# Kernel optimization log

Hardware: AMD Instinct MI355X
Metric: run time of the kernel (lower is better)

## Reference

```python
import jax, jax.numpy as jnp
import numpy as np

EMBED_DIM = 1024
HEAD_NUM = 16
HEAD_DIM = EMBED_DIM // HEAD_NUM
T, B, S = 2048, 4, 2048


def setup_inputs() -> dict:
    key = jax.random.key(0)
    ks = jax.random.split(key, 11)
    s = 0.02
    return {
        "query": jax.random.normal(ks[0], (T, B, EMBED_DIM), jnp.float32),
        "key": jax.random.normal(ks[1], (S, B, EMBED_DIM), jnp.float32),
        "value": jax.random.normal(ks[2], (S, B, EMBED_DIM), jnp.float32),
        "q_proj_weight": jax.random.normal(ks[3], (EMBED_DIM, EMBED_DIM), jnp.float32) * s,
        "k_proj_weight": jax.random.normal(ks[4], (EMBED_DIM, EMBED_DIM), jnp.float32) * s,
        "v_proj_weight": jax.random.normal(ks[5], (EMBED_DIM, EMBED_DIM), jnp.float32) * s,
        "in_proj_bias": jax.random.normal(ks[6], (3 * EMBED_DIM,), jnp.float32) * s,
        "bias_k": jax.random.normal(ks[7], (1, 1, EMBED_DIM), jnp.float32) * s,
        "bias_v": jax.random.normal(ks[8], (1, 1, EMBED_DIM), jnp.float32) * s,
        "out_proj_weight": jax.random.normal(ks[9], (EMBED_DIM, EMBED_DIM), jnp.float32) * s,
        "out_proj_bias": jax.random.normal(ks[10], (EMBED_DIM,), jnp.float32) * s,
    }


def reference(query, key, value, q_proj_weight, k_proj_weight, v_proj_weight,
              in_proj_bias, bias_k, bias_v, out_proj_weight, out_proj_bias):
    t, b, e = query.shape
    h, hd = HEAD_NUM, HEAD_DIM
    scaling = float(hd) ** -0.5
    # input projections (F.linear: x @ W.T + b)
    q = (query @ q_proj_weight.T + in_proj_bias[:e]) * scaling          # [T,B,E]
    k = key @ k_proj_weight.T + in_proj_bias[e:2 * e]                   # [S,B,E]
    v = value @ v_proj_weight.T + in_proj_bias[2 * e:]                  # [S,B,E]
    # append bias_k / bias_v token along the sequence dim
    k = jnp.concatenate([k, jnp.broadcast_to(bias_k, (1, b, e))], axis=0)  # [S+1,B,E]
    v = jnp.concatenate([v, jnp.broadcast_to(bias_v, (1, b, e))], axis=0)  # [S+1,B,E]
    # split heads: [L, B, E] -> [B*H, L, hd]
    q = q.reshape(t, b * h, hd).transpose(1, 0, 2)
    k = k.reshape(-1, b * h, hd).transpose(1, 0, 2)
    v = v.reshape(-1, b * h, hd).transpose(1, 0, 2)
    # full O(T*S) attention, as in the original bmm->softmax->bmm
    weights = jax.nn.softmax(jnp.einsum('nqd,nkd->nqk', q, k), axis=-1)  # [B*H,T,S+1]
    out = jnp.einsum('nqk,nkd->nqd', weights, v)                         # [B*H,T,hd]
    out = out.transpose(1, 0, 2).reshape(t, b, e)
    out = out @ out_proj_weight.T + out_proj_bias
    avg_weights = weights.sum(axis=1) / h                                # [B*H,S+1]
    return out, avg_weights
```

## Files before the change

kernel.cpp:

```cpp
#include <hip/hip_runtime.h>

#define T_DIM 2048
#define B_DIM 4
#define S_DIM 2048
#define E_DIM 1024
#define H_NUM 16
#define HD    64
#define NH    64
#define SP1   2049
#define SPAD  2112
#define NCHUNK 33
#define NTOKE ((size_t)T_DIM * B_DIM * E_DIM)

typedef short bf16x8 __attribute__((ext_vector_type(8)));
typedef short bf16x4 __attribute__((ext_vector_type(4)));
typedef float f32x4  __attribute__((ext_vector_type(4)));
typedef float f32x16 __attribute__((ext_vector_type(16)));
typedef unsigned int u32;

#define QSCALE 0.18033688011112042f

#if __has_builtin(__builtin_amdgcn_exp2f)
__device__ __forceinline__ float exp2_fast(float x) { return __builtin_amdgcn_exp2f(x); }
#else
__device__ __forceinline__ float exp2_fast(float x) { return __expf(x * 0.6931471805599453f); }
#endif

__device__ __forceinline__ unsigned short f2bf(float x) {
    union { float f; unsigned int u; } v; v.f = x;
    unsigned int r = v.u + 0x7FFFu + ((v.u >> 16) & 1u);
    return (unsigned short)(r >> 16);
}

__device__ __forceinline__ u32 cvtpk_bf16(float lo, float hi) {
    u32 r;
    asm("v_cvt_pk_bf16_f32 %0, %1, %2" : "=v"(r) : "v"(lo), "v"(hi));
    return r;
}
__device__ __forceinline__ void plswap(u32& a, u32& b) {
    asm("v_permlane32_swap_b32 %0, %1" : "+v"(a), "+v"(b));
}

__device__ __forceinline__ void load_lds16(const void* g, void* l) {
    __builtin_amdgcn_global_load_lds(
        (const __attribute__((address_space(1))) unsigned int*)g,
        (__attribute__((address_space(3))) unsigned int*)l, 16, 0, 0);
}

__global__ __launch_bounds__(256)
void cvt_all(const float* __restrict__ q, const float* __restrict__ k,
             const float* __restrict__ v, const float* __restrict__ w0,
             const float* __restrict__ w1, const float* __restrict__ w2,
             const float* __restrict__ w3, short* __restrict__ indst,
             short* __restrict__ wdst, short* __restrict__ k_h,
             short* __restrict__ v_h, const float* __restrict__ bias_k,
             const float* __restrict__ bias_v)
{
    const int y = blockIdx.y;
    if (y < 3) {
        const float* src = (y == 0) ? q : (y == 1) ? k : v;
        short* d = indst + (size_t)y * NTOKE;
        const size_t i = (size_t)blockIdx.x * 256 + threadIdx.x;
        const float4* s = reinterpret_cast<const float4*>(src) + i * 2;
        float4 a = s[0], b = s[1];
        uint4 o;
        o.x = cvtpk_bf16(a.x, a.y); o.y = cvtpk_bf16(a.z, a.w);
        o.z = cvtpk_bf16(b.x, b.y); o.w = cvtpk_bf16(b.z, b.w);
        *(reinterpret_cast<uint4*>(d) + i) = o;
    } else {
        const size_t gi = (size_t)blockIdx.x * 256 + threadIdx.x;
        const size_t per = (size_t)E_DIM * E_DIM / 8;
        if (gi < 4 * per) {
            const int wsel = (int)(gi / per);
            const size_t i = gi % per;
            const float* src = (wsel == 0) ? w0 : (wsel == 1) ? w1 : (wsel == 2) ? w2 : w3;
            short* d = wdst + (size_t)wsel * E_DIM * E_DIM;
            const float4* s = reinterpret_cast<const float4*>(src) + i * 2;
            float4 a = s[0], b = s[1];
            uint4 o;
            o.x = cvtpk_bf16(a.x, a.y); o.y = cvtpk_bf16(a.z, a.w);
            o.z = cvtpk_bf16(b.x, b.y); o.w = cvtpk_bf16(b.z, b.w);
            *(reinterpret_cast<uint4*>(d) + i) = o;
        } else {
            const size_t fi = gi - 4 * per;
            if (fi < (size_t)(SPAD - S_DIM) * NH * HD) {
                const int d   = (int)(fi & 63);
                const int row = (int)((fi >> 6) & 63);
                const int n   = (int)(fi >> 12);
                short bk = 0, bv = 0;
                if (row == 0) {
                    bk = (short)f2bf(bias_k[(n & 15) * HD + d]);
                    bv = (short)f2bf(bias_v[(n & 15) * HD + d]);
                }
                const size_t idx = ((size_t)n * SPAD + S_DIM + row) * HD + d;
                k_h[idx] = bk;
                v_h[idx] = bv;
            }
        }
    }
}

template<int MODE>
__global__ __launch_bounds__(256, 4)
void gemm_bf16(const short* __restrict__ Abase, const short* __restrict__ Wall,
               const float* __restrict__ biasAll, void* __restrict__ outp)
{
    __shared__ short As[128][64];
    __shared__ short Bs[128][64];
    const int bm = blockIdx.x, bn = blockIdx.y;
    const int z = (MODE == 0) ? blockIdx.z : 0;
    const short* Az = Abase + (MODE == 0 ? (size_t)z * NTOKE : 0);
    const short* W  = Wall + (size_t)z * E_DIM * E_DIM;
    const float* bias = biasAll + z * E_DIM;

    const int tid = threadIdx.x;
    const int l = tid & 63, w = tid >> 6;
    const int wr = w >> 1, wc = w & 1;
    const int lr = l & 15, lg = l >> 4;
    const int srow = tid >> 3, scol = (tid & 7) * 8;

    f32x4 acc[4][4] = {};

    for (int k0 = 0; k0 < E_DIM; k0 += 64) {
#pragma unroll
        for (int r = 0; r < 4; ++r) {
            const int row = r * 32 + srow;
            const short* ga;
            if (MODE == 3) {
                const int m = bm * 128 + row;
                ga = Az + ((size_t)((m & 3) * 16 + (k0 >> 6)) * T_DIM + (m >> 2)) * HD + scol;
            } else {
                ga = Az + (size_t)(bm * 128 + row) * E_DIM + k0 + scol;
            }
            load_lds16(ga, &As[row][scol]);
            load_lds16(W + (size_t)(bn * 128 + row) * E_DIM + k0 + scol, &Bs[row][scol]);
        }
        __syncthreads();

        __builtin_amdgcn_s_setprio(1);
#pragma unroll
        for (int c = 0; c < 2; ++c) {
            bf16x8 af[4], bf[4];
#pragma unroll
            for (int mi = 0; mi < 4; ++mi)
                af[mi] = *reinterpret_cast<const bf16x8*>(&As[wr * 64 + mi * 16 + lr][c * 32 + lg * 8]);
#pragma unroll
            for (int ni = 0; ni < 4; ++ni)
                bf[ni] = *reinterpret_cast<const bf16x8*>(&Bs[wc * 64 + ni * 16 + lr][c * 32 + lg * 8]);
#pragma unroll
            for (int mi = 0; mi < 4; ++mi)
#pragma unroll
                for (int ni = 0; ni < 4; ++ni)
                    acc[mi][ni] = __builtin_amdgcn_mfma_f32_16x16x32_bf16(
                        af[mi], bf[ni], acc[mi][ni], 0, 0, 0);
        }
        __builtin_amdgcn_s_setprio(0);
        __syncthreads();
    }

#pragma unroll
    for (int mi = 0; mi < 4; ++mi)
#pragma unroll
        for (int ni = 0; ni < 4; ++ni) {
            const int colg = bn * 128 + wc * 64 + ni * 16 + lr;
            const float bv = bias[colg];
#pragma unroll
            for (int r = 0; r < 4; ++r) {
                const int m = bm * 128 + wr * 64 + mi * 16 + lg * 4 + r;
                float v = acc[mi][ni][r] + bv;
                if (MODE == 3) {
                    ((float*)outp)[(size_t)m * E_DIM + colg] = v;
                } else {
                    if (z == 0) v *= QSCALE;
                    const int seq = m >> 2, b = m & 3;
                    const int head = colg >> 6, d = colg & 63;
                    const int sd = (z == 0) ? T_DIM : SPAD;
                    short* ob = (short*)outp;
                    if (z == 1) ob += (size_t)NH * T_DIM * HD;
                    else if (z == 2) ob += (size_t)NH * T_DIM * HD + (size_t)NH * SPAD * HD;
                    ob[((size_t)(b * 16 + head) * sd + seq) * HD + d] = (short)f2bf(v);
                }
            }
        }
}

__global__ __launch_bounds__(512, 4)
void attn_mfma(const short* __restrict__ q_h, const short* __restrict__ k_h,
               const short* __restrict__ v_h, short* __restrict__ o_h,
               float* __restrict__ m_arr, float* __restrict__ l_arr)
{
    __shared__ short KsD[2][64 * 64];
    __shared__ short VtD[2][64 * 64];

    const int id = blockIdx.x;
    const int xcd = id & 7, slot = id >> 3;
    const int n = xcd * 8 + (slot >> 3);
    const int q0 = (slot & 7) * 256;

    const int tid = threadIdx.x, l = tid & 63, w = tid >> 6;
    const int ql = l & 31;
    const int hi = l >> 5;
    const int qrow = q0 + w * 32 + ql;

    const int krow = tid >> 3, kcg = tid & 7;
    const int kswz = (kcg * 16) ^ ((krow & 7) << 4);
    const int sp = tid & 31, dq = tid >> 5;

    const short* kbase = k_h + (size_t)n * SPAD * HD;
    const short* vbase = v_h + (size_t)n * SPAD * HD;

    bf16x8 aq0, aq1, aq2, aq3;
    {
        const short* qp = q_h + ((size_t)n * T_DIM + qrow) * HD + hi * 8;
        aq0 = *(const bf16x8*)(qp);
        aq1 = *(const bf16x8*)(qp + 16);
        aq2 = *(const bf16x8*)(qp + 32);
        aq3 = *(const bf16x8*)(qp + 48);
    }

    bf16x8 pk  = *(const bf16x8*)(kbase + (size_t)krow * HD + kcg * 8);
    bf16x4 pva = *(const bf16x4*)(vbase + (size_t)(2 * sp) * HD + dq * 4);
    bf16x4 pvb = *(const bf16x4*)(vbase + (size_t)(2 * sp + 1) * HD + dq * 4);
    {
        char* KsB = (char*)KsD[0];
        char* VtB = (char*)VtD[0];
        *(bf16x8*)(KsB + krow * 128 + kswz) = pk;
#pragma unroll
        for (int j = 0; j < 4; ++j) {
            u32 pkd = (u32)(unsigned short)pva[j] | ((u32)(unsigned short)pvb[j] << 16);
            const int d = dq * 4 + j;
            *(u32*)(VtB + d * 128 + ((4 * sp) ^ ((d & 7) << 4))) = pkd;
        }
    }
    __syncthreads();

    float m_run = 0.0f;
    float l_run = 0.0f;
    f32x16 accA, accB;
#pragma unroll
    for (int r = 0; r < 16; ++r) { accA[r] = 0.f; accB[r] = 0.f; }

    for (int kc = 0; kc < NCHUNK; ++kc) {
        const char* KsB = (const char*)KsD[kc & 1];
        const char* VtB = (const char*)VtD[kc & 1];
        const bool more = (kc + 1 < NCHUNK);

        if (more) {
            const int s0n = (kc + 1) * 64;
            pk  = *(const bf16x8*)(kbase + (size_t)(s0n + krow) * HD + kcg * 8);
            pva = *(const bf16x4*)(vbase + (size_t)(s0n + 2 * sp) * HD + dq * 4);
            pvb = *(const bf16x4*)(vbase + (size_t)(s0n + 2 * sp + 1) * HD + dq * 4);
        }

        f32x16 sc0, sc1;
        const float nm = -m_run;
#pragma unroll
        for (int r = 0; r < 16; ++r) { sc0[r] = nm; sc1[r] = nm; }
        __builtin_amdgcn_s_setprio(1);
#pragma unroll
        for (int sl = 0; sl < 4; ++sl) {
            const int cb = ((sl * 32) + hi * 16) ^ ((ql & 7) << 4);
            bf16x8 kf0 = *(const bf16x8*)(KsB + ql * 128 + cb);
            bf16x8 kf1 = *(const bf16x8*)(KsB + (32 + ql) * 128 + cb);
            bf16x8 qf = (sl == 0) ? aq0 : (sl == 1) ? aq1 : (sl == 2) ? aq2 : aq3;
            sc0 = __builtin_amdgcn_mfma_f32_32x32x16_bf16(kf0, qf, sc0, 0, 0, 0);
            sc1 = __builtin_amdgcn_mfma_f32_32x32x16_bf16(kf1, qf, sc1, 0, 0, 0);
        }
        __builtin_amdgcn_s_setprio(0);

        const int s0 = kc * 64;
        if (s0 + 64 > SP1) {
#pragma unroll
            for (int r = 0; r < 16; ++r) {
                const int key = (r & 3) + 8 * (r >> 2) + 4 * hi;
                if (s0 + key >= SP1)      sc0[r] = -1e30f;
                if (s0 + 32 + key >= SP1) sc1[r] = -1e30f;
            }
        }

        float mv[16];
#pragma unroll
        for (int r = 0; r < 16; ++r) mv[r] = fmaxf(sc0[r], sc1[r]);
#pragma unroll
        for (int s = 8; s > 0; s >>= 1)
#pragma unroll
            for (int r = 0; r < s; ++r) mv[r] = fmaxf(mv[r], mv[r + s]);
        const float mx = fmaxf(mv[0], __shfl_xor(mv[0], 32));
        if (!__all(mx <= 8.0f)) {
            const float sh = fmaxf(mx, 0.0f);
            const float fac = exp2_fast(-sh);
            l_run *= fac;
#pragma unroll
            for (int r = 0; r < 16; ++r) {
                accA[r] *= fac; accB[r] *= fac;
                sc0[r] -= sh;   sc1[r] -= sh;
            }
            m_run += sh;
        }
        float p0[16], p1[16];
#pragma unroll
        for (int r = 0; r < 16; ++r) p0[r] = exp2_fast(sc0[r]);
#pragma unroll
        for (int r = 0; r < 16; ++r) p1[r] = exp2_fast(sc1[r]);
        float sv[16];
#pragma unroll
        for (int r = 0; r < 16; ++r) sv[r] = p0[r] + p1[r];
#pragma unroll
        for (int s = 8; s > 0; s >>= 1)
#pragma unroll
            for (int r = 0; r < s; ++r) sv[r] += sv[r + s];
        l_run += sv[0] + __shfl_xor(sv[0], 32);

        union PF { u32 u[4]; bf16x8 v; };
        PF pf0, pf1, pf2, pf3;
        {
            u32 a0 = cvtpk_bf16(p0[0], p0[1]),   b0 = cvtpk_bf16(p0[4], p0[5]);   plswap(a0, b0);
            u32 a1 = cvtpk_bf16(p0[2], p0[3]),   b1 = cvtpk_bf16(p0[6], p0[7]);   plswap(a1, b1);
            u32 a2 = cvtpk_bf16(p0[8], p0[9]),   b2 = cvtpk_bf16(p0[12], p0[13]); plswap(a2, b2);
            u32 a3 = cvtpk_bf16(p0[10], p0[11]), b3 = cvtpk_bf16(p0[14], p0[15]); plswap(a3, b3);
            pf0.u[0] = a0; pf0.u[1] = a1; pf0.u[2] = b0; pf0.u[3] = b1;
            pf1.u[0] = a2; pf1.u[1] = a3; pf1.u[2] = b2; pf1.u[3] = b3;
            u32 c0 = cvtpk_bf16(p1[0], p1[1]),   d0_ = cvtpk_bf16(p1[4], p1[5]);   plswap(c0, d0_);
            u32 c1 = cvtpk_bf16(p1[2], p1[3]),   d1_ = cvtpk_bf16(p1[6], p1[7]);   plswap(c1, d1_);
            u32 c2 = cvtpk_bf16(p1[8], p1[9]),   d2_ = cvtpk_bf16(p1[12], p1[13]); plswap(c2, d2_);
            u32 c3 = cvtpk_bf16(p1[10], p1[11]), d3_ = cvtpk_bf16(p1[14], p1[15]); plswap(c3, d3_);
            pf2.u[0] = c0; pf2.u[1] = c1; pf2.u[2] = d0_; pf2.u[3] = d1_;
            pf3.u[0] = c2; pf3.u[1] = c3; pf3.u[2] = d2_; pf3.u[3] = d3_;
        }

        __builtin_amdgcn_s_setprio(1);
#pragma unroll
        for (int ksl = 0; ksl < 4; ++ksl) {
            const int cb = ((ksl * 32) + hi * 16) ^ ((ql & 7) << 4);
            bf16x8 vf0 = *(const bf16x8*)(VtB + ql * 128 + cb);
            bf16x8 vf1 = *(const bf16x8*)(VtB + (32 + ql) * 128 + cb);
            const bf16x8 pv = (ksl == 0) ? pf0.v : (ksl == 1) ? pf1.v : (ksl == 2) ? pf2.v : pf3.v;
            accA = __builtin_amdgcn_mfma_f32_32x32x16_bf16(vf0, pv, accA, 0, 0, 0);
            accB = __builtin_amdgcn_mfma_f32_32x32x16_bf16(vf1, pv, accB, 0, 0, 0);
        }
        __builtin_amdgcn_s_setprio(0);

        if (more) {
            char* KsN = (char*)KsD[(kc & 1) ^ 1];
            char* VtN = (char*)VtD[(kc & 1) ^ 1];
            *(bf16x8*)(KsN + krow * 128 + kswz) = pk;
#pragma unroll
            for (int j = 0; j < 4; ++j) {
                u32 pkd = (u32)(unsigned short)pva[j] | ((u32)(unsigned short)pvb[j] << 16);
                const int d = dq * 4 + j;
                *(u32*)(VtN + d * 128 + ((4 * sp) ^ ((d & 7) << 4))) = pkd;
            }
            __syncthreads();
        }
    }

    const float il = 1.0f / l_run;
    short* orow = o_h + ((size_t)n * T_DIM + qrow) * HD;
#pragma unroll
    for (int rq = 0; rq < 4; ++rq) {
        uint2 st;
        st.x = cvtpk_bf16(accA[rq * 4 + 0] * il, accA[rq * 4 + 1] * il);
        st.y = cvtpk_bf16(accA[rq * 4 + 2] * il, accA[rq * 4 + 3] * il);
        *(uint2*)(orow + rq * 8 + hi * 4) = st;
        uint2 st2;
        st2.x = cvtpk_bf16(accB[rq * 4 + 0] * il, accB[rq * 4 + 1] * il);
        st2.y = cvtpk_bf16(accB[rq * 4 + 2] * il, accB[rq * 4 + 3] * il);
        *(uint2*)(orow + 32 + rq * 8 + hi * 4) = st2;
    }
    if (hi == 0) {
        m_arr[n * T_DIM + qrow] = m_run;
        l_arr[n * T_DIM + qrow] = l_run;
    }
}

__global__ __launch_bounds__(256)
void colsum_mfma(const short* __restrict__ q_h, const short* __restrict__ k_h,
                 const float* __restrict__ m_arr, const float* __restrict__ l_arr,
                 float* __restrict__ avg_out)
{
    __shared__ short Qs[2][64][72];
    __shared__ float msh[2][64];
    __shared__ float lih[2][64];

    const int id = blockIdx.x;
    const int xcd = id & 7, slot = id >> 3;
    const int n = xcd * 8 + slot / 33;
    const int s0 = (slot % 33) * 64;

    const int tid = threadIdx.x, l = tid & 63, w = tid >> 6;
    const int lr = l & 15, lg = l >> 4;
    const int qr = tid >> 3, qcg = tid & 7;

    const short* qbase = q_h + (size_t)n * T_DIM * HD;

    bf16x8 ak[2];
#pragma unroll
    for (int c = 0; c < 2; ++c)
        ak[c] = *reinterpret_cast<const bf16x8*>(
            k_h + ((size_t)n * SPAD + s0 + w * 16 + lr) * HD + c * 32 + lg * 8);

    bf16x8 qa = *(const bf16x8*)(qbase + (size_t)qr * HD + qcg * 8);
    bf16x8 qb = *(const bf16x8*)(qbase + (size_t)(32 + qr) * HD + qcg * 8);
    float mlv = 0.f;
    if (tid < 64) mlv = m_arr[n * T_DIM + tid];
    else if (tid < 128) mlv = l_arr[n * T_DIM + tid - 64];
    *(bf16x8*)&Qs[0][qr][qcg * 8] = qa;
    *(bf16x8*)&Qs[0][32 + qr][qcg * 8] = qb;
    if (tid < 64) msh[0][tid] = mlv;
    else if (tid < 128) lih[0][tid - 64] = 1.0f / mlv;
    __syncthreads();

    float csum[4] = {0.f, 0.f, 0.f, 0.f};

    for (int it = 0; it < T_DIM / 64; ++it) {
        const int buf = it & 1;
        const bool more = (it + 1 < T_DIM / 64);
        if (more) {
            const int qo = (it + 1) * 64;
            qa = *(const bf16x8*)(qbase + (size_t)(qo + qr) * HD + qcg * 8);
            qb = *(const bf16x8*)(qbase + (size_t)(qo + 32 + qr) * HD + qcg * 8);
            if (tid < 64) mlv = m_arr[n * T_DIM + qo + tid];
            else if (tid < 128) mlv = l_arr[n * T_DIM + qo + tid - 64];
        }
        __builtin_amdgcn_s_setprio(1);
#pragma unroll
        for (int qt = 0; qt < 4; ++qt) {
            bf16x8 bq0 = *reinterpret_cast<const bf16x8*>(&Qs[buf][qt * 16 + lr][lg * 8]);
            bf16x8 bq1 = *reinterpret_cast<const bf16x8*>(&Qs[buf][qt * 16 + lr][32 + lg * 8]);
            const float mq = msh[buf][qt * 16 + lr];
            const float lq = lih[buf][qt * 16 + lr];
            f32x4 z;
#pragma unroll
            for (int r = 0; r < 4; ++r) z[r] = -mq;
            z = __builtin_amdgcn_mfma_f32_16x16x32_bf16(ak[0], bq0, z, 0, 0, 0);
            z = __builtin_amdgcn_mfma_f32_16x16x32_bf16(ak[1], bq1, z, 0, 0, 0);
#pragma unroll
            for (int r = 0; r < 4; ++r)
                csum[r] += exp2_fast(z[r]) * lq;
        }
        __builtin_amdgcn_s_setprio(0);
        if (more) {
            *(bf16x8*)&Qs[buf ^ 1][qr][qcg * 8] = qa;
            *(bf16x8*)&Qs[buf ^ 1][32 + qr][qcg * 8] = qb;
            if (tid < 64) msh[buf ^ 1][tid] = mlv;
            else if (tid < 128) lih[buf ^ 1][tid - 64] = 1.0f / mlv;
            __syncthreads();
        }
    }

#pragma unroll
    for (int r = 0; r < 4; ++r) {
        float v = csum[r];
        v += __shfl_xor(v, 1, 16);
        v += __shfl_xor(v, 2, 16);
        v += __shfl_xor(v, 4, 16);
        v += __shfl_xor(v, 8, 16);
        if (lr == 0) {
            const int key = s0 + w * 16 + lg * 4 + r;
            if (key < SP1) avg_out[(size_t)n * SP1 + key] = v * 0.0625f;
        }
    }
}

extern "C" void kernel_launch(void* const* d_in, const int* in_sizes, int n_in,
                              void* d_out, int out_size, void* d_ws, size_t ws_size,
                              hipStream_t stream)
{
    const float* query   = (const float*)d_in[0];
    const float* key     = (const float*)d_in[1];
    const float* value   = (const float*)d_in[2];
    const float* wq      = (const float*)d_in[3];
    const float* wk      = (const float*)d_in[4];
    const float* wv      = (const float*)d_in[5];
    const float* in_bias = (const float*)d_in[6];
    const float* bias_k  = (const float*)d_in[7];
    const float* bias_v  = (const float*)d_in[8];
    const float* wo      = (const float*)d_in[9];
    const float* out_b   = (const float*)d_in[10];
    float* out = (float*)d_out;

    short* wqb    = (short*)d_ws;
    short* wob    = wqb + (size_t)3 * E_DIM * E_DIM;
    short* qkv_bf = wqb + (size_t)4 * E_DIM * E_DIM;
    short* q_h = qkv_bf + 3 * NTOKE;
    short* k_h = q_h + (size_t)NH * T_DIM * HD;
    short* v_h = k_h + (size_t)NH * SPAD * HD;
    short* o_h = v_h + (size_t)NH * SPAD * HD;
    float* m_arr = (float*)(o_h + (size_t)NH * T_DIM * HD);
    float* l_arr = m_arr + (size_t)NH * T_DIM;

    const dim3 blk(256);
    hipLaunchKernelGGL(cvt_all, dim3(4096, 4), blk, 0, stream,
                       query, key, value, wq, wk, wv, wo, qkv_bf, wqb,
                       k_h, v_h, bias_k, bias_v);

    hipLaunchKernelGGL((gemm_bf16<0>), dim3(64, 8, 3), blk, 0, stream,
                       qkv_bf, wqb, in_bias, (void*)q_h);
    hipLaunchKernelGGL(attn_mfma, dim3(512), dim3(512), 0, stream,
                       q_h, k_h, v_h, o_h, m_arr, l_arr);
    hipLaunchKernelGGL(colsum_mfma, dim3(2112), blk, 0, stream,
                       q_h, k_h, m_arr, l_arr, out + (size_t)T_DIM * B_DIM * E_DIM);
    hipLaunchKernelGGL((gemm_bf16<3>), dim3(64, 8), blk, 0, stream,
                       o_h, wob, out_b, (void*)out);
}
```

Baseline: 281.0 us.

## Double-buffer QKV GEMM LDS and merge colsum with output projection launch

The QKV projection GEMM gets double-buffered LDS tiles, so the next K-slice loads while MFMAs run on the current one, and its launch bound drops to 2 blocks per CU. The column-sum kernel and the output projection GEMM are merged into one launch that picks its role by block index, so the two independent tail stages can run side by side on the GPU. The aim is to hide global-load latency in the GEMM and to remove a launch gap and tail underutilisation. The cost is double the LDS per GEMM block, which can lower occupancy, and a mixed grid whose block roles may be unevenly balanced.

New measurement: 315.2 us. 1.12x slower.

```diff
diff --git a/kernel.cpp b/kernel.cpp
--- a/kernel.cpp
+++ b/kernel.cpp
@@ -100,16 +100,15 @@
     }
 }
 
-template<int MODE>
-__global__ __launch_bounds__(256, 4)
-void gemm_bf16(const short* __restrict__ Abase, const short* __restrict__ Wall,
-               const float* __restrict__ biasAll, void* __restrict__ outp)
+__global__ __launch_bounds__(256, 2)
+void gemm_qkv(const short* __restrict__ Abase, const short* __restrict__ Wall,
+              const float* __restrict__ biasAll, short* __restrict__ outp)
 {
-    __shared__ short As[128][64];
-    __shared__ short Bs[128][64];
+    __shared__ short As[2][128][64];
+    __shared__ short Bs[2][128][64];
     const int bm = blockIdx.x, bn = blockIdx.y;
-    const int z = (MODE == 0) ? blockIdx.z : 0;
-    const short* Az = Abase + (MODE == 0 ? (size_t)z * NTOKE : 0);
+    const int z = blockIdx.z;
+    const short* Az = Abase + (size_t)z * NTOKE;
     const short* W  = Wall + (size_t)z * E_DIM * E_DIM;
     const float* bias = biasAll + z * E_DIM;
 
@@ -119,23 +118,23 @@
     const int lr = l & 15, lg = l >> 4;
     const int srow = tid >> 3, scol = (tid & 7) * 8;
 
-    f32x4 acc[4][4] = {};
-
-    for (int k0 = 0; k0 < E_DIM; k0 += 64) {
+    auto stage = [&](int b, int k0) {
 #pragma unroll
         for (int r = 0; r < 4; ++r) {
             const int row = r * 32 + srow;
-            const short* ga;
-            if (MODE == 3) {
-                const int m = bm * 128 + row;
-                ga = Az + ((size_t)((m & 3) * 16 + (k0 >> 6)) * T_DIM + (m >> 2)) * HD + scol;
-            } else {
-                ga = Az + (size_t)(bm * 128 + row) * E_DIM + k0 + scol;
-            }
-            load_lds16(ga, &As[row][scol]);
-            load_lds16(W + (size_t)(bn * 128 + row) * E_DIM + k0 + scol, &Bs[row][scol]);
-        }
-        __syncthreads();
+            load_lds16(Az + (size_t)(bm * 128 + row) * E_DIM + k0 + scol, &As[b][row][scol]);
+            load_lds16(W + (size_t)(bn * 128 + row) * E_DIM + k0 + scol, &Bs[b][row][scol]);
+        }
+    };
+
+    stage(0, 0);
+    __syncthreads();
+
+    f32x4 acc[4][4] = {};
+    int buf = 0;
+
+    for (int k0 = 0; k0 < E_DIM; k0 += 64) {
+        if (k0 + 64 < E_DIM) stage(buf ^ 1, k0 + 64);
 
         __builtin_amdgcn_s_setprio(1);
 #pragma unroll
@@ -143,10 +142,10 @@
             bf16x8 af[4], bf[4];
 #pragma unroll
             for (int mi = 0; mi < 4; ++mi)
-                af[mi] = *reinterpret_cast<const bf16x8*>(&As[wr * 64 + mi * 16 + lr][c * 32 + lg * 8]);
+                af[mi] = *reinterpret_cast<const bf16x8*>(&As[buf][wr * 64 + mi * 16 + lr][c * 32 + lg * 8]);
 #pragma unroll
             for (int ni = 0; ni < 4; ++ni)
-                bf[ni] = *reinterpret_cast<const bf16x8*>(&Bs[wc * 64 + ni * 16 + lr][c * 32 + lg * 8]);
+                bf[ni] = *reinterpret_cast<const bf16x8*>(&Bs[buf][wc * 64 + ni * 16 + lr][c * 32 + lg * 8]);
 #pragma unroll
             for (int mi = 0; mi < 4; ++mi)
 #pragma unroll
@@ -156,6 +155,7 @@
         }
         __builtin_amdgcn_s_setprio(0);
         __syncthreads();
+        buf ^= 1;
     }
 
 #pragma unroll
@@ -168,18 +168,14 @@
             for (int r = 0; r < 4; ++r) {
                 const int m = bm * 128 + wr * 64 + mi * 16 + lg * 4 + r;
                 float v = acc[mi][ni][r] + bv;
-                if (MODE == 3) {
-                    ((float*)outp)[(size_t)m * E_DIM + colg] = v;
-                } else {
-                    if (z == 0) v *= QSCALE;
-                    const int seq = m >> 2, b = m & 3;
-                    const int head = colg >> 6, d = colg & 63;
-                    const int sd = (z == 0) ? T_DIM : SPAD;
-                    short* ob = (short*)outp;
-                    if (z == 1) ob += (size_t)NH * T_DIM * HD;
-                    else if (z == 2) ob += (size_t)NH * T_DIM * HD + (size_t)NH * SPAD * HD;
-                    ob[((size_t)(b * 16 + head) * sd + seq) * HD + d] = (short)f2bf(v);
-                }
+                if (z == 0) v *= QSCALE;
+                const int seq = m >> 2, b = m & 3;
+                const int head = colg >> 6, d = colg & 63;
+                const int sd = (z == 0) ? T_DIM : SPAD;
+                short* ob = outp;
+                if (z == 1) ob += (size_t)NH * T_DIM * HD;
+                else if (z == 2) ob += (size_t)NH * T_DIM * HD + (size_t)NH * SPAD * HD;
+                ob[((size_t)(b * 16 + head) * sd + seq) * HD + d] = (short)f2bf(v);
             }
         }
 }
@@ -374,91 +370,157 @@
 }
 
 __global__ __launch_bounds__(256)
-void colsum_mfma(const short* __restrict__ q_h, const short* __restrict__ k_h,
-                 const float* __restrict__ m_arr, const float* __restrict__ l_arr,
-                 float* __restrict__ avg_out)
+void tail_fused(const short* __restrict__ q_h, const short* __restrict__ k_h,
+                const float* __restrict__ m_arr, const float* __restrict__ l_arr,
+                const short* __restrict__ o_h, const short* __restrict__ wob,
+                const float* __restrict__ out_b, float* __restrict__ out,
+                float* __restrict__ avg_out)
 {
-    __shared__ short Qs[2][64][72];
-    __shared__ float msh[2][64];
-    __shared__ float lih[2][64];
-
-    const int id = blockIdx.x;
-    const int xcd = id & 7, slot = id >> 3;
-    const int n = xcd * 8 + slot / 33;
-    const int s0 = (slot % 33) * 64;
-
-    const int tid = threadIdx.x, l = tid & 63, w = tid >> 6;
-    const int lr = l & 15, lg = l >> 4;
-    const int qr = tid >> 3, qcg = tid & 7;
-
-    const short* qbase = q_h + (size_t)n * T_DIM * HD;
-
-    bf16x8 ak[2];
-#pragma unroll
-    for (int c = 0; c < 2; ++c)
-        ak[c] = *reinterpret_cast<const bf16x8*>(
-            k_h + ((size_t)n * SPAD + s0 + w * 16 + lr) * HD + c * 32 + lg * 8);
-
-    bf16x8 qa = *(const bf16x8*)(qbase + (size_t)qr * HD + qcg * 8);
-    bf16x8 qb = *(const bf16x8*)(qbase + (size_t)(32 + qr) * HD + qcg * 8);
-    float mlv = 0.f;
-    if (tid < 64) mlv = m_arr[n * T_DIM + tid];
-    else if (tid < 128) mlv = l_arr[n * T_DIM + tid - 64];
-    *(bf16x8*)&Qs[0][qr][qcg * 8] = qa;
-    *(bf16x8*)&Qs[0][32 + qr][qcg * 8] = qb;
-    if (tid < 64) msh[0][tid] = mlv;
-    else if (tid < 128) lih[0][tid - 64] = 1.0f / mlv;
-    __syncthreads();
-
-    float csum[4] = {0.f, 0.f, 0.f, 0.f};
-
-    for (int it = 0; it < T_DIM / 64; ++it) {
-        const int buf = it & 1;
-        const bool more = (it + 1 < T_DIM / 64);
-        if (more) {
-            const int qo = (it + 1) * 64;
-            qa = *(const bf16x8*)(qbase + (size_t)(qo + qr) * HD + qcg * 8);
-            qb = *(const bf16x8*)(qbase + (size_t)(qo + 32 + qr) * HD + qcg * 8);
-            if (tid < 64) mlv = m_arr[n * T_DIM + qo + tid];
-            else if (tid < 128) mlv = l_arr[n * T_DIM + qo + tid - 64];
-        }
-        __builtin_amdgcn_s_setprio(1);
-#pragma unroll
-        for (int qt = 0; qt < 4; ++qt) {
-            bf16x8 bq0 = *reinterpret_cast<const bf16x8*>(&Qs[buf][qt * 16 + lr][lg * 8]);
-            bf16x8 bq1 = *reinterpret_cast<const bf16x8*>(&Qs[buf][qt * 16 + lr][32 + lg * 8]);
-            const float mq = msh[buf][qt * 16 + lr];
-            const float lq = lih[buf][qt * 16 + lr];
-            f32x4 z;
-#pragma unroll
-            for (int r = 0; r < 4; ++r) z[r] = -mq;
-            z = __builtin_amdgcn_mfma_f32_16x16x32_bf16(ak[0], bq0, z, 0, 0, 0);
-            z = __builtin_amdgcn_mfma_f32_16x16x32_bf16(ak[1], bq1, z, 0, 0, 0);
-#pragma unroll
-            for (int r = 0; r < 4; ++r)
-                csum[r] += exp2_fast(z[r]) * lq;
-        }
-        __builtin_amdgcn_s_setprio(0);
-        if (more) {
-            *(bf16x8*)&Qs[buf ^ 1][qr][qcg * 8] = qa;
-            *(bf16x8*)&Qs[buf ^ 1][32 + qr][qcg * 8] = qb;
-            if (tid < 64) msh[buf ^ 1][tid] = mlv;
-            else if (tid < 128) lih[buf ^ 1][tid - 64] = 1.0f / mlv;
+    __shared__ char smem[32768];
+    const int bid = blockIdx.x;
+    const int tid = threadIdx.x;
+
+    if (bid < 2112) {
+        short (*Qs)[64][72] = (short(*)[64][72])smem;
+        float* msh = (float*)(smem + 18432);
+        float* lih = msh + 128;
+
+        const int xcd = bid & 7, slot = bid >> 3;
+        const int n = xcd * 8 + slot / 33;
+        const int s0 = (slot % 33) * 64;
+
+        const int l = tid & 63, w = tid >> 6;
+        const int lr = l & 15, lg = l >> 4;
+        const int qr = tid >> 3, qcg = tid & 7;
+
+        const short* qbase = q_h + (size_t)n * T_DIM * HD;
+
+        bf16x8 ak[2];
+#pragma unroll
+        for (int c = 0; c < 2; ++c)
+            ak[c] = *reinterpret_cast<const bf16x8*>(
+                k_h + ((size_t)n * SPAD + s0 + w * 16 + lr) * HD + c * 32 + lg * 8);
+
+        bf16x8 qa = *(const bf16x8*)(qbase + (size_t)qr * HD + qcg * 8);
+        bf16x8 qb = *(const bf16x8*)(qbase + (size_t)(32 + qr) * HD + qcg * 8);
+        float mlv = 0.f;
+        if (tid < 64) mlv = m_arr[n * T_DIM + tid];
+        else if (tid < 128) mlv = l_arr[n * T_DIM + tid - 64];
+        *(bf16x8*)&Qs[0][qr][qcg * 8] = qa;
+        *(bf16x8*)&Qs[0][32 + qr][qcg * 8] = qb;
+        if (tid < 64) msh[tid] = mlv;
+        else if (tid < 128) lih[tid - 64] = 1.0f / mlv;
+        __syncthreads();
+
+        float csum[4] = {0.f, 0.f, 0.f, 0.f};
+
+        for (int it = 0; it < T_DIM / 64; ++it) {
+            const int buf = it & 1;
+            const bool more = (it + 1 < T_DIM / 64);
+            if (more) {
+                const int qo = (it + 1) * 64;
+                qa = *(const bf16x8*)(qbase + (size_t)(qo + qr) * HD + qcg * 8);
+                qb = *(const bf16x8*)(qbase + (size_t)(qo + 32 + qr) * HD + qcg * 8);
+                if (tid < 64) mlv = m_arr[n * T_DIM + qo + tid];
+                else if (tid < 128) mlv = l_arr[n * T_DIM + qo + tid - 64];
+            }
+            __builtin_amdgcn_s_setprio(1);
+#pragma unroll
+            for (int qt = 0; qt < 4; ++qt) {
+                bf16x8 bq0 = *reinterpret_cast<const bf16x8*>(&Qs[buf][qt * 16 + lr][lg * 8]);
+                bf16x8 bq1 = *reinterpret_cast<const bf16x8*>(&Qs[buf][qt * 16 + lr][32 + lg * 8]);
+                const float mq = msh[buf * 64 + qt * 16 + lr];
+                const float lq = lih[buf * 64 + qt * 16 + lr];
+                f32x4 z;
+#pragma unroll
+                for (int r = 0; r < 4; ++r) z[r] = -mq;
+                z = __builtin_amdgcn_mfma_f32_16x16x32_bf16(ak[0], bq0, z, 0, 0, 0);
+                z = __builtin_amdgcn_mfma_f32_16x16x32_bf16(ak[1], bq1, z, 0, 0, 0);
+#pragma unroll
+                for (int r = 0; r < 4; ++r)
+                    csum[r] += exp2_fast(z[r]) * lq;
+            }
+            __builtin_amdgcn_s_setprio(0);
+            if (more) {
+                *(bf16x8*)&Qs[buf ^ 1][qr][qcg * 8] = qa;
+                *(bf16x8*)&Qs[buf ^ 1][32 + qr][qcg * 8] = qb;
+                if (tid < 64) msh[(buf ^ 1) * 64 + tid] = mlv;
+                else if (tid < 128) lih[(buf ^ 1) * 64 + tid - 64] = 1.0f / mlv;
+                __syncthreads();
+            }
+        }
+
+#pragma unroll
+        for (int r = 0; r < 4; ++r) {
+            float v = csum[r];
+            v += __shfl_xor(v, 1, 16);
+            v += __shfl_xor(v, 2, 16);
+            v += __shfl_xor(v, 4, 16);
+            v += __shfl_xor(v, 8, 16);
+            if (lr == 0) {
+                const int key = s0 + w * 16 + lg * 4 + r;
+                if (key < SP1) avg_out[(size_t)n * SP1 + key] = v * 0.0625f;
+            }
+        }
+    } else {
+        short (*As)[64] = (short(*)[64])smem;
+        short (*Bs)[64] = (short(*)[64])(smem + 16384);
+
+        const int idx = bid - 2112;
+        const int bm = idx & 63, bn = idx >> 6;
+
+        const int l = tid & 63, w = tid >> 6;
+        const int wr = w >> 1, wc = w & 1;
+        const int lr = l & 15, lg = l >> 4;
+        const int srow = tid >> 3, scol = (tid & 7) * 8;
+
+        f32x4 acc[4][4] = {};
+
+        for (int k0 = 0; k0 < E_DIM; k0 += 64) {
+#pragma unroll
+            for (int r = 0; r < 4; ++r) {
+                const int row = r * 32 + srow;
+                const int m = bm * 128 + row;
+                const short* ga = o_h +
+                    ((size_t)((m & 3) * 16 + (k0 >> 6)) * T_DIM + (m >> 2)) * HD + scol;
+                load_lds16(ga, &As[row][scol]);
+                load_lds16(wob + (size_t)(bn * 128 + row) * E_DIM + k0 + scol, &Bs[row][scol]);
+            }
             __syncthreads();
-        }
-    }
-
-#pragma unroll
-    for (int r = 0; r < 4; ++r) {
-        float v = csum[r];
-        v += __shfl_xor(v, 1, 16);
-        v += __shfl_xor(v, 2, 16);
-        v += __shfl_xor(v, 4, 16);
-        v += __shfl_xor(v, 8, 16);
-        if (lr == 0) {
-            const int key = s0 + w * 16 + lg * 4 + r;
-            if (key < SP1) avg_out[(size_t)n * SP1 + key] = v * 0.0625f;
-        }
+
+            __builtin_amdgcn_s_setprio(1);
+#pragma unroll
+            for (int c = 0; c < 2; ++c) {
+                bf16x8 af[4], bf[4];
+#pragma unroll
+                for (int mi = 0; mi < 4; ++mi)
+                    af[mi] = *reinterpret_cast<const bf16x8*>(&As[wr * 64 + mi * 16 + lr][c * 32 + lg * 8]);
+#pragma unroll
+                for (int ni = 0; ni < 4; ++ni)
+                    bf[ni] = *reinterpret_cast<const bf16x8*>(&Bs[wc * 64 + ni * 16 + lr][c * 32 + lg * 8]);
+#pragma unroll
+                for (int mi = 0; mi < 4; ++mi)
+#pragma unroll
+                    for (int ni = 0; ni < 4; ++ni)
+                        acc[mi][ni] = __builtin_amdgcn_mfma_f32_16x16x32_bf16(
+                            af[mi], bf[ni], acc[mi][ni], 0, 0, 0);
+            }
+            __builtin_amdgcn_s_setprio(0);
+            __syncthreads();
+        }
+
+#pragma unroll
+        for (int mi = 0; mi < 4; ++mi)
+#pragma unroll
+            for (int ni = 0; ni < 4; ++ni) {
+                const int colg = bn * 128 + wc * 64 + ni * 16 + lr;
+                const float bv = out_b[colg];
+#pragma unroll
+                for (int r = 0; r < 4; ++r) {
+                    const int m = bm * 128 + wr * 64 + mi * 16 + lg * 4 + r;
+                    out[(size_t)m * E_DIM + colg] = acc[mi][ni][r] + bv;
+                }
+            }
     }
 }
 
@@ -494,12 +556,11 @@
                        query, key, value, wq, wk, wv, wo, qkv_bf, wqb,
                        k_h, v_h, bias_k, bias_v);
 
-    hipLaunchKernelGGL((gemm_bf16<0>), dim3(64, 8, 3), blk, 0, stream,
-                       qkv_bf, wqb, in_bias, (void*)q_h);
+    hipLaunchKernelGGL(gemm_qkv, dim3(64, 8, 3), blk, 0, stream,
+                       qkv_bf, wqb, in_bias, q_h);
     hipLaunchKernelGGL(attn_mfma, dim3(512), dim3(512), 0, stream,
                        q_h, k_h, v_h, o_h, m_arr, l_arr);
-    hipLaunchKernelGGL(colsum_mfma, dim3(2112), blk, 0, stream,
-                       q_h, k_h, m_arr, l_arr, out + (size_t)T_DIM * B_DIM * E_DIM);
-    hipLaunchKernelGGL((gemm_bf16<3>), dim3(64, 8), blk, 0, stream,
-                       o_h, wob, out_b, (void*)out);
-}
+    hipLaunchKernelGGL(tail_fused, dim3(2112 + 512), blk, 0, stream,
+                       q_h, k_h, m_arr, l_arr, o_h, wob, out_b,
+                       out, out + (size_t)T_DIM * B_DIM * E_DIM);
+}
```
